# Kernel tuning notes

Hardware: AMD Instinct MI355X
Metric: run time of the kernel (lower is better)

## Reference

```python
import jax, jax.numpy as jnp
import numpy as np

B, C, L = 8, 256, 8192
G, K = 64, 7  # weight channels (groups) and kernel size


def setup_inputs() -> dict:
    key = jax.random.key(0)
    k1, k2 = jax.random.split(key)
    x = jax.random.normal(k1, (B, C, L), dtype=jnp.float32)
    w = jax.random.normal(k2, (B, G, K, L), dtype=jnp.float32)
    return {"x": x, "w": w}


def reference(x, w):
    # x: [B, C, L]; w: [B, G, K, L]
    Bsz, Cin, Len = x.shape
    Gw, Ks = w.shape[1], w.shape[2]
    pad = (Ks - 1) // 2
    x_pad = jnp.pad(x, ((0, 0), (0, 0), (pad, pad)))  # zero pad, 'same' output
    # x_unfold[b, c, k, l] = x_pad[b, c, l + k]  -> [B, C, K, L]
    x_unfold = jnp.stack([x_pad[:, :, k:k + Len] for k in range(Ks)], axis=2)
    # each input channel c uses weight channel c % G (spatially adaptive kernel)
    group_idx = jnp.arange(Cin) % Gw
    w_exp = w[:, group_idx]  # [B, C, K, L]
    return (x_unfold * w_exp).sum(axis=2)  # [B, C, L]
```

## Files before the change

kernel.cpp:

```cpp
#include <hip/hip_runtime.h>


constexpr int Bn   = 8;
constexpr int Cn   = 256;
constexpr int Ln   = 8192;
constexpr int Gn   = 64;
constexpr int Kn   = 7;
constexpr int CPG  = Cn / Gn;
constexpr int LPT  = 4;
constexpr int BLOCK = 256;
constexpr int TILE_L = BLOCK * LPT;
constexpr int NTILE  = Ln / TILE_L;
constexpr size_t CH_STRIDE = (size_t)Gn * Ln;

__global__ __launch_bounds__(BLOCK, 4) void ska1d_kernel(
    const float* __restrict__ x,
    const float* __restrict__ w,
    float* __restrict__ out)
{
    const int bid   = blockIdx.x;
    const int ltile = bid % NTILE;
    const int g     = (bid / NTILE) % Gn;
    const int b     = bid / (NTILE * Gn);
    const int l0    = ltile * TILE_L + (int)threadIdx.x * LPT;

    const float* wp = w   + ((size_t)(b * Gn + g) * Kn) * Ln + l0;
    const float* xp = x   + ((size_t)b * Cn + g) * Ln + l0;
    float*       op = out + ((size_t)b * Cn + g) * Ln + l0;

    const bool has_lo = (l0 >= 4);
    const bool has_hi = (l0 + LPT < Ln);
    const float4 z = make_float4(0.f, 0.f, 0.f, 0.f);

    float4 W[Kn];
#pragma unroll
    for (int k = 0; k < Kn; ++k)
        W[k] = *reinterpret_cast<const float4*>(wp + (size_t)k * Ln);

    float4 A[CPG], Bv[CPG], Cv[CPG];
#pragma unroll
    for (int j = 0; j < CPG; ++j) {
        const float* xj = xp + j * CH_STRIDE;
        A[j]  = has_lo ? *reinterpret_cast<const float4*>(xj - 4) : z;
        Bv[j] = *reinterpret_cast<const float4*>(xj);
        Cv[j] = has_hi ? *reinterpret_cast<const float4*>(xj + 4) : z;
    }

    __builtin_amdgcn_sched_barrier(0);

#pragma unroll
    for (int j = 0; j < CPG; ++j) {
        float xs[12];
        xs[0] = A[j].x;  xs[1] = A[j].y;  xs[2]  = A[j].z;  xs[3]  = A[j].w;
        xs[4] = Bv[j].x; xs[5] = Bv[j].y; xs[6]  = Bv[j].z; xs[7]  = Bv[j].w;
        xs[8] = Cv[j].x; xs[9] = Cv[j].y; xs[10] = Cv[j].z; xs[11] = Cv[j].w;

        float4 o;
        float* opx = &o.x;
        const float* Wf = &W[0].x;
#pragma unroll
        for (int i = 0; i < 4; ++i) {
            float acc = 0.f;
#pragma unroll
            for (int k = 0; k < Kn; ++k)
                acc = fmaf(xs[1 + i + k], Wf[k * 4 + i], acc);
            opx[i] = acc;
        }
        *reinterpret_cast<float4*>(op + j * CH_STRIDE) = o;
    }
}

extern "C" void kernel_launch(void* const* d_in, const int* in_sizes, int n_in,
                              void* d_out, int out_size, void* d_ws, size_t ws_size,
                              hipStream_t stream)
{
    const float* x = (const float*)d_in[0];
    const float* w = (const float*)d_in[1];
    float* out     = (float*)d_out;

    const int grid = Bn * Gn * NTILE;
    ska1d_kernel<<<grid, BLOCK, 0, stream>>>(x, w, out);
}
```

Before: 225.9 us.

## Make blocks loop over half the sequence with double-buffered register prefetch

```diff
diff --git a/kernel.cpp b/kernel.cpp
--- a/kernel.cpp
+++ b/kernel.cpp
@@ -1,72 +1,91 @@
 #include <hip/hip_runtime.h>
 
 
-constexpr int Bn   = 8;
-constexpr int Cn   = 256;
-constexpr int Ln   = 8192;
-constexpr int Gn   = 64;
-constexpr int Kn   = 7;
-constexpr int CPG  = Cn / Gn;
-constexpr int LPT  = 4;
+constexpr int Bn = 8, Cn = 256, Ln = 8192, Gn = 64, Kn = 7;
 constexpr int BLOCK = 256;
-constexpr int TILE_L = BLOCK * LPT;
-constexpr int NTILE  = Ln / TILE_L;
-constexpr size_t CH_STRIDE = (size_t)Gn * Ln;
+constexpr int CHUNK = 256;
+constexpr int ITERS = (Ln / 2) / CHUNK;
+
+__device__ __forceinline__ float4 ld4(const float* p) {
+    return *reinterpret_cast<const float4*>(p);
+}
+
+struct Frag {
+    float4 W0, W1, W2, W3, W4, W5, W6;
+    float4 A, B, C;
+};
+
+__device__ __forceinline__ void load_frag(Frag& f, const float* wp,
+                                          const float* xp, int lg) {
+    f.W0 = ld4(wp);
+    f.W1 = ld4(wp + Ln);
+    f.W2 = ld4(wp + 2 * Ln);
+    f.W3 = ld4(wp + 3 * Ln);
+    f.W4 = ld4(wp + 4 * Ln);
+    f.W5 = ld4(wp + 5 * Ln);
+    f.W6 = ld4(wp + 6 * Ln);
+    const float4 z = make_float4(0.f, 0.f, 0.f, 0.f);
+    f.A = (lg >= 4)      ? ld4(xp - 4) : z;
+    f.B =                  ld4(xp);
+    f.C = (lg + 4 < Ln)  ? ld4(xp + 4) : z;
+}
+
+__device__ __forceinline__ void compute_store(const Frag& f, float* op) {
+    float xs[12];
+    xs[0] = f.A.x; xs[1] = f.A.y; xs[2]  = f.A.z; xs[3]  = f.A.w;
+    xs[4] = f.B.x; xs[5] = f.B.y; xs[6]  = f.B.z; xs[7]  = f.B.w;
+    xs[8] = f.C.x; xs[9] = f.C.y; xs[10] = f.C.z; xs[11] = f.C.w;
+    const float* Wf = &f.W0.x;
+    float4 o;
+    float* opx = &o.x;
+#pragma unroll
+    for (int i = 0; i < 4; ++i) {
+        float acc = 0.f;
+#pragma unroll
+        for (int k = 0; k < Kn; ++k)
+            acc = fmaf(xs[1 + i + k], Wf[k * 4 + i], acc);
+        opx[i] = acc;
+    }
+    *reinterpret_cast<float4*>(op) = o;
+}
 
 __global__ __launch_bounds__(BLOCK, 4) void ska1d_kernel(
     const float* __restrict__ x,
     const float* __restrict__ w,
     float* __restrict__ out)
 {
-    const int bid   = blockIdx.x;
-    const int ltile = bid % NTILE;
-    const int g     = (bid / NTILE) % Gn;
-    const int b     = bid / (NTILE * Gn);
-    const int l0    = ltile * TILE_L + (int)threadIdx.x * LPT;
+    const int bid  = blockIdx.x;
+    const int half = bid & 1;
+    const int g    = (bid >> 1) & (Gn - 1);
+    const int b    = bid >> 7;
+    const int wv   = (int)threadIdx.x >> 6;
+    const int lane = (int)threadIdx.x & 63;
+    const int c    = g + wv * Gn;
+    const int l0   = half * (Ln / 2) + lane * 4;
 
     const float* wp = w   + ((size_t)(b * Gn + g) * Kn) * Ln + l0;
-    const float* xp = x   + ((size_t)b * Cn + g) * Ln + l0;
-    float*       op = out + ((size_t)b * Cn + g) * Ln + l0;
+    const float* xp = x   + ((size_t)(b * Cn + c)) * Ln + l0;
+    float*       op = out + ((size_t)(b * Cn + c)) * Ln + l0;
 
-    const bool has_lo = (l0 >= 4);
-    const bool has_hi = (l0 + LPT < Ln);
-    const float4 z = make_float4(0.f, 0.f, 0.f, 0.f);
+    Frag f0, f1;
+    load_frag(f0, wp, xp, l0);
 
-    float4 W[Kn];
-#pragma unroll
-    for (int k = 0; k < Kn; ++k)
-        W[k] = *reinterpret_cast<const float4*>(wp + (size_t)k * Ln);
+    for (int it = 0; it < ITERS; it += 2) {
+        {
+            const int nidx = (it + 1 < ITERS) ? it + 1 : it;
+            const int off  = nidx * CHUNK;
+            load_frag(f1, wp + off, xp + off, l0 + off);
+        }
+        __builtin_amdgcn_sched_barrier(0);
+        compute_store(f0, op + it * CHUNK);
 
-    float4 A[CPG], Bv[CPG], Cv[CPG];
-#pragma unroll
-    for (int j = 0; j < CPG; ++j) {
-        const float* xj = xp + j * CH_STRIDE;
-        A[j]  = has_lo ? *reinterpret_cast<const float4*>(xj - 4) : z;
-        Bv[j] = *reinterpret_cast<const float4*>(xj);
-        Cv[j] = has_hi ? *reinterpret_cast<const float4*>(xj + 4) : z;
-    }
-
-    __builtin_amdgcn_sched_barrier(0);
-
-#pragma unroll
-    for (int j = 0; j < CPG; ++j) {
-        float xs[12];
-        xs[0] = A[j].x;  xs[1] = A[j].y;  xs[2]  = A[j].z;  xs[3]  = A[j].w;
-        xs[4] = Bv[j].x; xs[5] = Bv[j].y; xs[6]  = Bv[j].z; xs[7]  = Bv[j].w;
-        xs[8] = Cv[j].x; xs[9] = Cv[j].y; xs[10] = Cv[j].z; xs[11] = Cv[j].w;
-
-        float4 o;
-        float* opx = &o.x;
-        const float* Wf = &W[0].x;
-#pragma unroll
-        for (int i = 0; i < 4; ++i) {
-            float acc = 0.f;
-#pragma unroll
-            for (int k = 0; k < Kn; ++k)
-                acc = fmaf(xs[1 + i + k], Wf[k * 4 + i], acc);
-            opx[i] = acc;
+        {
+            const int nidx = (it + 2 < ITERS) ? it + 2 : ITERS - 1;
+            const int off  = nidx * CHUNK;
+            load_frag(f0, wp + off, xp + off, l0 + off);
         }
-        *reinterpret_cast<float4*>(op + j * CH_STRIDE) = o;
+        __builtin_amdgcn_sched_barrier(0);
+        compute_store(f1, op + (it + 1) * CHUNK);
     }
 }
 
@@ -78,6 +97,6 @@
     const float* w = (const float*)d_in[1];
     float* out     = (float*)d_out;
 
-    const int grid = Bn * Gn * NTILE;
+    const int grid = Bn * Gn * 2;
     ska1d_kernel<<<grid, BLOCK, 0, stream>>>(x, w, out);
 }
```

Result: slower. 233.3 us (+3.2%).
